# Kernel tuning notes

Measured on AMD Instinct MI355X. Metric: run time of the kernel, lower is better.

The kernel has to match this reference:

```python
import jax, jax.numpy as jnp
import numpy as np

N, E, F_IN, H, D = 50000, 800000, 128, 4, 32


def setup_inputs() -> dict:
    key = jax.random.key(0)
    k1, k2, k3, k4 = jax.random.split(key, 4)
    feat = jax.random.normal(k1, (N, F_IN), dtype=jnp.float32)
    src = jax.random.randint(k2, (E,), 0, N, dtype=jnp.int64)
    dst = jax.random.randint(k3, (E,), 0, N, dtype=jnp.int64)
    # fc weight (xavier-normal-ish scale) and explicit bias
    W = jax.random.normal(k4, (F_IN, H * D), dtype=jnp.float32) * (1.0 / np.sqrt(F_IN))
    bias = jnp.zeros((H * D,), dtype=jnp.float32)
    return {"feat": feat, "src": src, "dst": dst, "W": W, "bias": bias}


def reference(feat, src, dst, W, bias):
    # fc projection, view as (N, H, D)
    ft = (feat @ W).reshape(N, H, D)
    # apply_edges u_dot_v: per-edge per-head dot product -> [E, H]
    e = jnp.einsum("ehd,ehd->eh", ft[src], ft[dst])
    # edge_softmax over incoming edges of each dst node (numerically stable)
    emax = jax.ops.segment_max(e, dst, num_segments=N)  # [N, H]
    ex = jnp.exp(e - emax[dst])
    denom = jax.ops.segment_sum(ex, dst, num_segments=N)  # [N, H]
    a = ex / denom[dst]  # [E, H]
    # update_all: u_mul_e + sum -> weighted scatter aggregation
    msg = ft[src] * a[:, :, None]  # [E, H, D]
    rst = jax.ops.segment_sum(msg, dst, num_segments=N)  # [N, H, D]
    return rst + bias.reshape(1, H, D)
```

## Files before the change

kernel.cpp:

```cpp
#include <hip/hip_runtime.h>
#include <math.h>

#define F 128
#define HEADS 4
#define DHEAD 32
#define HIST_H 128
#define CW_MAX 6592

typedef unsigned short ushort_t;
typedef __attribute__((ext_vector_type(8))) short short8;
typedef __attribute__((ext_vector_type(4))) float f32x4;

__device__ __forceinline__ ushort_t f2bf(float x) {
  unsigned u = __float_as_uint(x);
  unsigned r = u + 0x7FFFu + ((u >> 16) & 1u);
  return (ushort_t)(r >> 16);
}

__device__ __forceinline__ void unpack8(const int4& r, float* v) {
  int rr[4] = {r.x, r.y, r.z, r.w};
#pragma unroll
  for (int q = 0; q < 4; q++) {
    unsigned u = (unsigned)rr[q];
    v[2 * q] = __uint_as_float(u << 16);
    v[2 * q + 1] = __uint_as_float(u & 0xFFFF0000u);
  }
}

__global__ __launch_bounds__(256) void wprep_kernel(
    const float* __restrict__ W, ushort_t* __restrict__ whi,
    ushort_t* __restrict__ wlo) {
  int idx = blockIdx.x * 256 + threadIdx.x;
  if (idx >= 128 * 128) return;
  int j = idx & 7;
  int lane = (idx >> 3) & 63;
  int f = idx >> 9;
  int kt = f >> 3, nt = f & 7;
  int k = kt * 32 + (lane >> 4) * 8 + j;
  int n = nt * 16 + (lane & 15);
  float w = W[k * 128 + n];
  unsigned u = __float_as_uint(w);
  unsigned hb = u & 0xFFFF0000u;
  float lo = w - __uint_as_float(hb);
  whi[idx] = (ushort_t)(hb >> 16);
  wlo[idx] = f2bf(lo);
}

__global__ __launch_bounds__(256) void gemm_hist_kernel(
    const float* __restrict__ feat, const ushort_t* __restrict__ whi,
    const ushort_t* __restrict__ wlo, ushort_t* __restrict__ ftb, int N,
    const int* __restrict__ dst, ushort_t* __restrict__ partials, int cwp,
    int E, int gemmBlocks) {
  __shared__ int lh[CW_MAX];
  if ((int)blockIdx.x >= gemmBlocks) {
    const int hb = blockIdx.x - gemmBlocks;
    const int cls = hb & 7;
    const int h = hb >> 3;
    const int cw = (N + 7) >> 3;
    const int nbase = cls * cw;
    for (int j = threadIdx.x; j < cw; j += 256) lh[j] = 0;
    __syncthreads();
    const int seg = (E + HIST_H - 1) / HIST_H;
    const int e0 = h * seg;
    const int e1 = min(e0 + seg, E);
    int e = e0 + (int)threadIdx.x;
    for (; e + 768 < e1; e += 1024) {
      int d0 = dst[e];
      int d1 = dst[e + 256];
      int d2 = dst[e + 512];
      int d3 = dst[e + 768];
      if ((unsigned)(d0 - nbase) < (unsigned)cw) atomicAdd(&lh[d0 - nbase], 1);
      if ((unsigned)(d1 - nbase) < (unsigned)cw) atomicAdd(&lh[d1 - nbase], 1);
      if ((unsigned)(d2 - nbase) < (unsigned)cw) atomicAdd(&lh[d2 - nbase], 1);
      if ((unsigned)(d3 - nbase) < (unsigned)cw) atomicAdd(&lh[d3 - nbase], 1);
    }
    for (; e < e1; e += 256) {
      int d = dst[e];
      if ((unsigned)(d - nbase) < (unsigned)cw) atomicAdd(&lh[d - nbase], 1);
    }
    __syncthreads();
    ushort_t* prow = partials + (size_t)(cls * HIST_H + h) * cwp;
    for (int j = threadIdx.x; j < cw; j += 256) prow[j] = (ushort_t)lh[j];
    return;
  }
  const int t = threadIdx.x;
  const int wv = t >> 6;
  const int l = t & 63;
  const int g = l >> 4;
  const int lm = l & 15;
  const int arow = blockIdx.x * 64 + wv * 16 + lm;
  const int arowc = min(arow, N - 1);

  f32x4 acc[8];
#pragma unroll
  for (int nt = 0; nt < 8; nt++) acc[nt] = (f32x4){0.f, 0.f, 0.f, 0.f};

#pragma unroll
  for (int kt = 0; kt < 4; kt++) {
    const float* ap = feat + (size_t)arowc * F + kt * 32 + g * 8;
    float a[8];
    *(float4*)&a[0] = *(const float4*)ap;
    *(float4*)&a[4] = *(const float4*)(ap + 4);
    short8 ahi, alo;
#pragma unroll
    for (int j = 0; j < 8; j++) {
      unsigned u = __float_as_uint(a[j]);
      unsigned hb2 = u & 0xFFFF0000u;
      float lo = a[j] - __uint_as_float(hb2);
      ahi[j] = (short)(hb2 >> 16);
      alo[j] = (short)f2bf(lo);
    }
    const ushort_t* bh = whi + (size_t)(kt * 8) * 512 + l * 8;
    const ushort_t* bl = wlo + (size_t)(kt * 8) * 512 + l * 8;
#pragma unroll
    for (int nt = 0; nt < 8; nt++) {
      short8 bhi = *(const short8*)(bh + nt * 512);
      short8 blo = *(const short8*)(bl + nt * 512);
      acc[nt] =
          __builtin_amdgcn_mfma_f32_16x16x32_bf16(ahi, blo, acc[nt], 0, 0, 0);
      acc[nt] =
          __builtin_amdgcn_mfma_f32_16x16x32_bf16(alo, bhi, acc[nt], 0, 0, 0);
      acc[nt] =
          __builtin_amdgcn_mfma_f32_16x16x32_bf16(ahi, bhi, acc[nt], 0, 0, 0);
    }
  }

  const int orow0 = blockIdx.x * 64 + wv * 16 + g * 4;
#pragma unroll
  for (int reg = 0; reg < 4; reg++) {
    int orow = orow0 + reg;
    if (orow < N) {
#pragma unroll
      for (int nt = 0; nt < 8; nt++)
        ftb[(size_t)orow * F + nt * 16 + lm] = f2bf(acc[nt][reg]);
    }
  }
}

__global__ void scan_block_kernel(const ushort_t* __restrict__ partials,
                                  int cwp, int* __restrict__ offs,
                                  ushort_t* __restrict__ rel16,
                                  int* __restrict__ bsums, int N) {
  __shared__ int s[256];
  int t = threadIdx.x, i = blockIdx.x * 256 + t;
  int v = 0;
  if (i < N) {
    int cw = (N + 7) >> 3;
    int c = i / cw;
    int j = i - c * cw;
    const ushort_t* pb = partials + (size_t)c * HIST_H * cwp + j;
    ushort_t* cb = rel16 + (size_t)c * HIST_H * cwp + j;
    int run = 0;
#pragma unroll 8
    for (int h = 0; h < HIST_H; h++) {
      cb[(size_t)h * cwp] = (ushort_t)run;
      run += pb[(size_t)h * cwp];
    }
    v = run;
  }
  s[t] = v;
  __syncthreads();
  for (int d = 1; d < 256; d <<= 1) {
    int x = (t >= d) ? s[t - d] : 0;
    __syncthreads();
    s[t] += x;
    __syncthreads();
  }
  if (i < N) offs[i] = s[t] - v;
  if (t == 255) bsums[blockIdx.x] = s[255];
}

__global__ void scan_finish_kernel(int* __restrict__ offs,
                                   const int* __restrict__ bsums, int N,
                                   int E) {
  int t = threadIdx.x, b = blockIdx.x;
  int v = (t < b) ? bsums[t] : 0;
#pragma unroll
  for (int d = 32; d > 0; d >>= 1) v += __shfl_down(v, d, 64);
  __shared__ int wsum[4];
  if ((t & 63) == 0) wsum[t >> 6] = v;
  __syncthreads();
  int total = wsum[0] + wsum[1] + wsum[2] + wsum[3];
  int i = b * 256 + t;
  if (i < N) offs[i] += total;
  if (b == 0 && t == 0) offs[N] = E;
}

__global__ __launch_bounds__(256) void scatter_kernel(
    const int* __restrict__ src, const int* __restrict__ dst,
    const int* __restrict__ offs, const ushort_t* __restrict__ rel16, int cwp,
    int* __restrict__ csr, int E, int N) {
  __shared__ int lcur[CW_MAX];
  const int cls = blockIdx.x & 7;
  const int h = blockIdx.x >> 3;
  const int cw = (N + 7) >> 3;
  const int nbase = cls * cw;
  const int jmax = min(cw, N - nbase);
  const ushort_t* crow = rel16 + (size_t)(cls * HIST_H + h) * cwp;
  for (int j = threadIdx.x; j < jmax; j += 256)
    lcur[j] = offs[nbase + j] + (int)crow[j];
  __syncthreads();
  const int seg = (E + HIST_H - 1) / HIST_H;
  const int e0 = h * seg;
  const int e1 = min(e0 + seg, E);
  int e = e0 + (int)threadIdx.x;
  for (; e + 768 < e1; e += 1024) {
    int d0 = dst[e];
    int d1 = dst[e + 256];
    int d2 = dst[e + 512];
    int d3 = dst[e + 768];
    int s0 = src[e];
    int s1 = src[e + 256];
    int s2 = src[e + 512];
    int s3 = src[e + 768];
    if ((unsigned)(d0 - nbase) < (unsigned)cw)
      csr[atomicAdd(&lcur[d0 - nbase], 1)] = s0;
    if ((unsigned)(d1 - nbase) < (unsigned)cw)
      csr[atomicAdd(&lcur[d1 - nbase], 1)] = s1;
    if ((unsigned)(d2 - nbase) < (unsigned)cw)
      csr[atomicAdd(&lcur[d2 - nbase], 1)] = s2;
    if ((unsigned)(d3 - nbase) < (unsigned)cw)
      csr[atomicAdd(&lcur[d3 - nbase], 1)] = s3;
  }
  for (; e < e1; e += 256) {
    int d = dst[e];
    int sv = src[e];
    if ((unsigned)(d - nbase) < (unsigned)cw)
      csr[atomicAdd(&lcur[d - nbase], 1)] = sv;
  }
}

__global__ __launch_bounds__(256) void aggregate_kernel(
    const ushort_t* __restrict__ ftb, const int* __restrict__ offs,
    const int* __restrict__ csr, const float* __restrict__ bias,
    float* __restrict__ out, int N) {
  const int T = blockIdx.x * 256 + threadIdx.x;
  if (T >= N * 16) return;
  const int sub = T & 3;
  const int p = T >> 2;
  const int h = p & 3;
  const int n = p >> 2;
  const int dimBase = h * DHEAD + sub * 8;

  const int off = offs[n];
  const int deg = offs[n + 1] - off;

  const float LOG2E = 1.4426950408889634f;
  float ftd[8];
  {
    int4 r = *(const int4*)&ftb[n * F + dimBase];
    unpack8(r, ftd);
#pragma unroll
    for (int j = 0; j < 8; j++) ftd[j] *= LOG2E;
  }

  float s = 0.f;
  float acc[8];
#pragma unroll
  for (int j = 0; j < 8; j++) acc[j] = 0.f;

#define PROCESS(RX)                                              \
  do {                                                           \
    float v[8];                                                  \
    unpack8(RX, v);                                              \
    float part = 0.f;                                            \
    _Pragma("unroll") for (int j = 0; j < 8; j++) part =         \
        fmaf(ftd[j], v[j], part);                                \
    part += __shfl_xor(part, 1, 4);                              \
    part += __shfl_xor(part, 2, 4);                              \
    float w = exp2f(part);                                       \
    s += w;                                                      \
    _Pragma("unroll") for (int j = 0; j < 8; j++) acc[j] =       \
        fmaf(w, v[j], acc[j]);                                   \
  } while (0)

  int4 R0 = make_int4(0, 0, 0, 0), R1 = R0, R2 = R0, R3 = R0;
  if (deg > 0) {
    int dm1 = deg - 1;
    int s0 = csr[off];
    int s1 = csr[off + min(1, dm1)];
    int s2 = csr[off + min(2, dm1)];
    int s3 = csr[off + min(3, dm1)];
    R0 = *(const int4*)&ftb[s0 * F + dimBase];
    R1 = *(const int4*)&ftb[s1 * F + dimBase];
    R2 = *(const int4*)&ftb[s2 * F + dimBase];
    R3 = *(const int4*)&ftb[s3 * F + dimBase];
  }
  int i = 0;
  for (; i + 4 <= deg; i += 4) {
    int dm1 = deg - 1;
    int sa = csr[off + min(i + 4, dm1)];
    int sb = csr[off + min(i + 5, dm1)];
    int sc = csr[off + min(i + 6, dm1)];
    int sd = csr[off + min(i + 7, dm1)];
    int4 Na = *(const int4*)&ftb[sa * F + dimBase];
    int4 Nb = *(const int4*)&ftb[sb * F + dimBase];
    int4 Nc = *(const int4*)&ftb[sc * F + dimBase];
    int4 Nd = *(const int4*)&ftb[sd * F + dimBase];
    PROCESS(R0);
    PROCESS(R1);
    PROCESS(R2);
    PROCESS(R3);
    R0 = Na; R1 = Nb; R2 = Nc; R3 = Nd;
  }
  int r = deg - i;
  if (r > 0) PROCESS(R0);
  if (r > 1) PROCESS(R1);
  if (r > 2) PROCESS(R2);
#undef PROCESS

  float inv = (deg > 0) ? 1.f / s : 0.f;
  float4 b0 = *(const float4*)&bias[dimBase];
  float4 b1 = *(const float4*)&bias[dimBase + 4];
  f32x4 o0 = {acc[0] * inv + b0.x, acc[1] * inv + b0.y, acc[2] * inv + b0.z,
              acc[3] * inv + b0.w};
  f32x4 o1 = {acc[4] * inv + b1.x, acc[5] * inv + b1.y, acc[6] * inv + b1.z,
              acc[7] * inv + b1.w};
  __builtin_nontemporal_store(o0, (f32x4*)&out[n * F + dimBase]);
  __builtin_nontemporal_store(o1, (f32x4*)&out[n * F + dimBase + 4]);
}

extern "C" void kernel_launch(void* const* d_in, const int* in_sizes, int n_in,
                              void* d_out, int out_size, void* d_ws,
                              size_t ws_size, hipStream_t stream) {
  const float* feat = (const float*)d_in[0];
  const int* src = (const int*)d_in[1];
  const int* dst = (const int*)d_in[2];
  const float* W = (const float*)d_in[3];
  const float* bias = (const float*)d_in[4];
  float* out = (float*)d_out;

  const int N = in_sizes[0] / F;
  const int E = in_sizes[1];
  const int cw = (N + 7) >> 3;
  const int cwp = (cw + 31) & ~31;

  char* ws = (char*)d_ws;
  ushort_t* ftb = (ushort_t*)ws;
  size_t ftB = (size_t)N * F * sizeof(ushort_t);
  ftB = (ftB + 255) & ~(size_t)255;
  int* offs = (int*)(ws + ftB);
  int* bsums = offs + N + 1;
  int* csr = bsums + 256;
  ushort_t* whi = (ushort_t*)(csr + E);
  ushort_t* wlo = whi + 128 * 128;
  ushort_t* partials = wlo + 128 * 128;
  ushort_t* rel16 = partials + 8 * HIST_H * cwp;

  wprep_kernel<<<64, 256, 0, stream>>>(W, whi, wlo);

  int gemmBlocks = (N + 63) / 64;
  gemm_hist_kernel<<<gemmBlocks + 8 * HIST_H, 256, 0, stream>>>(
      feat, whi, wlo, ftb, N, dst, partials, cwp, E, gemmBlocks);

  int nb = (N + 255) / 256;
  scan_block_kernel<<<nb, 256, 0, stream>>>(partials, cwp, offs, rel16,
                                            bsums, N);
  scan_finish_kernel<<<nb, 256, 0, stream>>>(offs, bsums, N, E);

  scatter_kernel<<<8 * HIST_H, 256, 0, stream>>>(src, dst, offs, rel16, cwp,
                                                 csr, E, N);

  aggregate_kernel<<<(N * 16 + 255) / 256, 256, 0, stream>>>(ftb, offs, csr,
                                                             bias, out, N);
}
```

Measured before the change: 86.11 us.

## Store CSR source indices as 16-bit and halve the dst partition classes

The CSR neighbour list now stores source node ids as unsigned shorts instead of ints. This halves the bytes the scatter kernel writes and the aggregate kernel reads. The number of destination-range classes drops from 8 to 4, so the histogram and scatter kernels read the dst/src arrays half as many times. In exchange, each block's LDS histogram doubles to about 52 KB, which lowers occupancy. The 16-bit indices are only correct while N stays below 65536.

```diff
diff --git a/kernel.cpp b/kernel.cpp
--- a/kernel.cpp
+++ b/kernel.cpp
@@ -4,8 +4,9 @@
 #define F 128
 #define HEADS 4
 #define DHEAD 32
+#define CLS 4
 #define HIST_H 128
-#define CW_MAX 6592
+#define CW_MAX 13184
 
 typedef unsigned short ushort_t;
 typedef __attribute__((ext_vector_type(8))) short short8;
@@ -54,9 +55,9 @@
   __shared__ int lh[CW_MAX];
   if ((int)blockIdx.x >= gemmBlocks) {
     const int hb = blockIdx.x - gemmBlocks;
-    const int cls = hb & 7;
-    const int h = hb >> 3;
-    const int cw = (N + 7) >> 3;
+    const int cls = hb & (CLS - 1);
+    const int h = hb >> 2;
+    const int cw = (N + CLS - 1) / CLS;
     const int nbase = cls * cw;
     for (int j = threadIdx.x; j < cw; j += 256) lh[j] = 0;
     __syncthreads();
@@ -145,7 +146,7 @@
   int t = threadIdx.x, i = blockIdx.x * 256 + t;
   int v = 0;
   if (i < N) {
-    int cw = (N + 7) >> 3;
+    int cw = (N + CLS - 1) / CLS;
     int c = i / cw;
     int j = i - c * cw;
     const ushort_t* pb = partials + (size_t)c * HIST_H * cwp + j;
@@ -189,11 +190,11 @@
 __global__ __launch_bounds__(256) void scatter_kernel(
     const int* __restrict__ src, const int* __restrict__ dst,
     const int* __restrict__ offs, const ushort_t* __restrict__ rel16, int cwp,
-    int* __restrict__ csr, int E, int N) {
+    ushort_t* __restrict__ csr, int E, int N) {
   __shared__ int lcur[CW_MAX];
-  const int cls = blockIdx.x & 7;
-  const int h = blockIdx.x >> 3;
-  const int cw = (N + 7) >> 3;
+  const int cls = blockIdx.x & (CLS - 1);
+  const int h = blockIdx.x >> 2;
+  const int cw = (N + CLS - 1) / CLS;
   const int nbase = cls * cw;
   const int jmax = min(cw, N - nbase);
   const ushort_t* crow = rel16 + (size_t)(cls * HIST_H + h) * cwp;
@@ -214,25 +215,25 @@
     int s2 = src[e + 512];
     int s3 = src[e + 768];
     if ((unsigned)(d0 - nbase) < (unsigned)cw)
-      csr[atomicAdd(&lcur[d0 - nbase], 1)] = s0;
+      csr[atomicAdd(&lcur[d0 - nbase], 1)] = (ushort_t)s0;
     if ((unsigned)(d1 - nbase) < (unsigned)cw)
-      csr[atomicAdd(&lcur[d1 - nbase], 1)] = s1;
+      csr[atomicAdd(&lcur[d1 - nbase], 1)] = (ushort_t)s1;
     if ((unsigned)(d2 - nbase) < (unsigned)cw)
-      csr[atomicAdd(&lcur[d2 - nbase], 1)] = s2;
+      csr[atomicAdd(&lcur[d2 - nbase], 1)] = (ushort_t)s2;
     if ((unsigned)(d3 - nbase) < (unsigned)cw)
-      csr[atomicAdd(&lcur[d3 - nbase], 1)] = s3;
+      csr[atomicAdd(&lcur[d3 - nbase], 1)] = (ushort_t)s3;
   }
   for (; e < e1; e += 256) {
     int d = dst[e];
     int sv = src[e];
     if ((unsigned)(d - nbase) < (unsigned)cw)
-      csr[atomicAdd(&lcur[d - nbase], 1)] = sv;
+      csr[atomicAdd(&lcur[d - nbase], 1)] = (ushort_t)sv;
   }
 }
 
 __global__ __launch_bounds__(256) void aggregate_kernel(
     const ushort_t* __restrict__ ftb, const int* __restrict__ offs,
-    const int* __restrict__ csr, const float* __restrict__ bias,
+    const ushort_t* __restrict__ csr, const float* __restrict__ bias,
     float* __restrict__ out, int N) {
   const int T = blockIdx.x * 256 + threadIdx.x;
   if (T >= N * 16) return;
@@ -281,10 +282,10 @@
     int s1 = csr[off + min(1, dm1)];
     int s2 = csr[off + min(2, dm1)];
     int s3 = csr[off + min(3, dm1)];
-    R0 = *(const int4*)&ftb[s0 * F + dimBase];
-    R1 = *(const int4*)&ftb[s1 * F + dimBase];
-    R2 = *(const int4*)&ftb[s2 * F + dimBase];
-    R3 = *(const int4*)&ftb[s3 * F + dimBase];
+    R0 = *(const int4*)&ftb[(size_t)s0 * F + dimBase];
+    R1 = *(const int4*)&ftb[(size_t)s1 * F + dimBase];
+    R2 = *(const int4*)&ftb[(size_t)s2 * F + dimBase];
+    R3 = *(const int4*)&ftb[(size_t)s3 * F + dimBase];
   }
   int i = 0;
   for (; i + 4 <= deg; i += 4) {
@@ -293,10 +294,10 @@
     int sb = csr[off + min(i + 5, dm1)];
     int sc = csr[off + min(i + 6, dm1)];
     int sd = csr[off + min(i + 7, dm1)];
-    int4 Na = *(const int4*)&ftb[sa * F + dimBase];
-    int4 Nb = *(const int4*)&ftb[sb * F + dimBase];
-    int4 Nc = *(const int4*)&ftb[sc * F + dimBase];
-    int4 Nd = *(const int4*)&ftb[sd * F + dimBase];
+    int4 Na = *(const int4*)&ftb[(size_t)sa * F + dimBase];
+    int4 Nb = *(const int4*)&ftb[(size_t)sb * F + dimBase];
+    int4 Nc = *(const int4*)&ftb[(size_t)sc * F + dimBase];
+    int4 Nd = *(const int4*)&ftb[(size_t)sd * F + dimBase];
     PROCESS(R0);
     PROCESS(R1);
     PROCESS(R2);
@@ -332,7 +333,7 @@
 
   const int N = in_sizes[0] / F;
   const int E = in_sizes[1];
-  const int cw = (N + 7) >> 3;
+  const int cw = (N + CLS - 1) / CLS;
   const int cwp = (cw + 31) & ~31;
 
   char* ws = (char*)d_ws;
@@ -341,16 +342,16 @@
   ftB = (ftB + 255) & ~(size_t)255;
   int* offs = (int*)(ws + ftB);
   int* bsums = offs + N + 1;
-  int* csr = bsums + 256;
-  ushort_t* whi = (ushort_t*)(csr + E);
+  ushort_t* csr = (ushort_t*)(bsums + 256);
+  ushort_t* whi = csr + ((E + 128) & ~127);
   ushort_t* wlo = whi + 128 * 128;
   ushort_t* partials = wlo + 128 * 128;
-  ushort_t* rel16 = partials + 8 * HIST_H * cwp;
+  ushort_t* rel16 = partials + CLS * HIST_H * cwp;
 
   wprep_kernel<<<64, 256, 0, stream>>>(W, whi, wlo);
 
   int gemmBlocks = (N + 63) / 64;
-  gemm_hist_kernel<<<gemmBlocks + 8 * HIST_H, 256, 0, stream>>>(
+  gemm_hist_kernel<<<gemmBlocks + CLS * HIST_H, 256, 0, stream>>>(
       feat, whi, wlo, ftb, N, dst, partials, cwp, E, gemmBlocks);
 
   int nb = (N + 255) / 256;
@@ -358,8 +359,8 @@
                                             bsums, N);
   scan_finish_kernel<<<nb, 256, 0, stream>>>(offs, bsums, N, E);
 
-  scatter_kernel<<<8 * HIST_H, 256, 0, stream>>>(src, dst, offs, rel16, cwp,
-                                                 csr, E, N);
+  scatter_kernel<<<CLS * HIST_H, 256, 0, stream>>>(src, dst, offs, rel16, cwp,
+                                                   csr, E, N);
 
   aggregate_kernel<<<(N * 16 + 255) / 256, 256, 0, stream>>>(ftb, offs, csr,
                                                              bias, out, N);
```

Result: no change. 85.62 us (-0.6%).
